# Kernel tuning notes

Measured on AMD Instinct MI355X. Metric: run time of the kernel, lower is better.

## Reference

```python
import jax, jax.numpy as jnp
import numpy as np

EPS = 1e-5  # torch nn.LayerNorm default

def setup_inputs() -> dict:
    key = jax.random.key(0)
    k1, k2 = jax.random.split(key)
    x = jax.random.normal(k1, (8388608, 4), dtype=jnp.float32)
    W = jax.random.normal(k2, (4, 3), dtype=jnp.float32)
    gamma = jnp.ones((4,), dtype=jnp.float32)
    beta = jnp.zeros((4,), dtype=jnp.float32)
    return {"x": x, "W": W, "gamma": gamma, "beta": beta}

def reference(x, W, gamma, beta):
    # LayerNorm over last dim (size 4)
    mu = jnp.mean(x, axis=-1, keepdims=True)
    var = jnp.mean(jnp.square(x - mu), axis=-1, keepdims=True)
    h = (x - mu) * jax.lax.rsqrt(var + EPS) * gamma + beta
    # small linear (4 -> 3) then softmax over last dim
    logits = h @ W  # [N, 3]
    return jax.nn.softmax(logits, axis=-1)
```

## Files before the change

### kernel.cpp

```cpp
#include <hip/hip_runtime.h>

#define LN_EPS 1e-5f

__global__ __launch_bounds__(256) void ln_linear_softmax_kernel(
    const float4* __restrict__ x,
    const float*  __restrict__ W,
    const float*  __restrict__ gamma,
    const float*  __restrict__ beta,
    float*        __restrict__ out,
    int n)
{
    int row = blockIdx.x * blockDim.x + threadIdx.x;
    if (row >= n) return;

    float4 v = x[row];

    float mu = (v.x + v.y + v.z + v.w) * 0.25f;
    float dx = v.x - mu, dy = v.y - mu, dz = v.z - mu, dw = v.w - mu;
    float var = (dx*dx + dy*dy + dz*dz + dw*dw) * 0.25f;
    float rs = rsqrtf(var + LN_EPS);

    float4 g = *(const float4*)gamma;
    float4 b = *(const float4*)beta;
    float h0 = dx * rs * g.x + b.x;
    float h1 = dy * rs * g.y + b.y;
    float h2 = dz * rs * g.z + b.z;
    float h3 = dw * rs * g.w + b.w;

    const float4* W4 = (const float4*)W;
    float4 w0 = W4[0];
    float4 w1 = W4[1];
    float4 w2 = W4[2];

    float l0 = h0*w0.x + h1*w0.w + h2*w1.z + h3*w2.y;
    float l1 = h0*w0.y + h1*w1.x + h2*w1.w + h3*w2.z;
    float l2 = h0*w0.z + h1*w1.y + h2*w2.x + h3*w2.w;

    float m  = fmaxf(l0, fmaxf(l1, l2));
    float e0 = __expf(l0 - m);
    float e1 = __expf(l1 - m);
    float e2 = __expf(l2 - m);
    float inv = 1.0f / (e0 + e1 + e2);

    float* o = out + (size_t)row * 3;
    o[0] = e0 * inv;
    o[1] = e1 * inv;
    o[2] = e2 * inv;
}

extern "C" void kernel_launch(void* const* d_in, const int* in_sizes, int n_in,
                              void* d_out, int out_size, void* d_ws, size_t ws_size,
                              hipStream_t stream) {
    const float* x     = (const float*)d_in[0];
    const float* W     = (const float*)d_in[1];
    const float* gamma = (const float*)d_in[2];
    const float* beta  = (const float*)d_in[3];
    float* out = (float*)d_out;

    int n = in_sizes[0] / 4;
    int block = 256;
    int grid = (n + block - 1) / block;
    ln_linear_softmax_kernel<<<grid, block, 0, stream>>>(
        (const float4*)x, W, gamma, beta, out, n);
}
```

Before: 215.8 us.

## Stage outputs in LDS for coalesced float4 stores, four rows per thread, nontemporal access

Each thread now handles four rows and writes its three softmax outputs into shared memory. After a barrier, the block writes the staged results out as fully coalesced 16-byte nontemporal stores, replacing the scattered 3-float strided stores. Input loads are also marked nontemporal. The aim is to cut partial-cacheline write traffic in this memory-bound kernel. The cost is LDS usage, a barrier, and the requirement that n*3 be divisible by 4 to handle the output tail correctly.

```diff
diff --git a/kernel.cpp b/kernel.cpp
--- a/kernel.cpp
+++ b/kernel.cpp
@@ -2,50 +2,77 @@
 
 #define LN_EPS 1e-5f
 
-__global__ __launch_bounds__(256) void ln_linear_softmax_kernel(
-    const float4* __restrict__ x,
-    const float*  __restrict__ W,
-    const float*  __restrict__ gamma,
-    const float*  __restrict__ beta,
-    float*        __restrict__ out,
+typedef float v4f __attribute__((ext_vector_type(4)));
+
+constexpr int BLOCK = 256;
+constexpr int RPT   = 4;
+constexpr int RPB   = BLOCK * RPT;
+
+__global__ __launch_bounds__(BLOCK) void ln_linear_softmax_kernel(
+    const v4f*   __restrict__ x,
+    const float* __restrict__ W,
+    const float* __restrict__ gamma,
+    const float* __restrict__ beta,
+    v4f*         __restrict__ out4,
     int n)
 {
-    int row = blockIdx.x * blockDim.x + threadIdx.x;
-    if (row >= n) return;
+    __shared__ float lds[RPB * 3];
 
-    float4 v = x[row];
+    const int  tid  = threadIdx.x;
+    const long base = (long)blockIdx.x * RPB;
 
-    float mu = (v.x + v.y + v.z + v.w) * 0.25f;
-    float dx = v.x - mu, dy = v.y - mu, dz = v.z - mu, dw = v.w - mu;
-    float var = (dx*dx + dy*dy + dz*dz + dw*dw) * 0.25f;
-    float rs = rsqrtf(var + LN_EPS);
+    const v4f g = *(const v4f*)gamma;
+    const v4f b = *(const v4f*)beta;
+    const v4f* W4 = (const v4f*)W;
+    const v4f w0 = W4[0];
+    const v4f w1 = W4[1];
+    const v4f w2 = W4[2];
 
-    float4 g = *(const float4*)gamma;
-    float4 b = *(const float4*)beta;
-    float h0 = dx * rs * g.x + b.x;
-    float h1 = dy * rs * g.y + b.y;
-    float h2 = dz * rs * g.z + b.z;
-    float h3 = dw * rs * g.w + b.w;
+    #pragma unroll
+    for (int k = 0; k < RPT; ++k) {
+        const int  rl  = tid + k * BLOCK;
+        const long row = base + rl;
+        if (row < n) {
+            v4f v = __builtin_nontemporal_load(&x[row]);
 
-    const float4* W4 = (const float4*)W;
-    float4 w0 = W4[0];
-    float4 w1 = W4[1];
-    float4 w2 = W4[2];
+            float mu = (v.x + v.y + v.z + v.w) * 0.25f;
+            float dx = v.x - mu, dy = v.y - mu, dz = v.z - mu, dw = v.w - mu;
+            float var = (dx*dx + dy*dy + dz*dz + dw*dw) * 0.25f;
+            float rs  = rsqrtf(var + LN_EPS);
 
-    float l0 = h0*w0.x + h1*w0.w + h2*w1.z + h3*w2.y;
-    float l1 = h0*w0.y + h1*w1.x + h2*w1.w + h3*w2.z;
-    float l2 = h0*w0.z + h1*w1.y + h2*w2.x + h3*w2.w;
+            float h0 = dx * rs * g.x + b.x;
+            float h1 = dy * rs * g.y + b.y;
+            float h2 = dz * rs * g.z + b.z;
+            float h3 = dw * rs * g.w + b.w;
 
-    float m  = fmaxf(l0, fmaxf(l1, l2));
-    float e0 = __expf(l0 - m);
-    float e1 = __expf(l1 - m);
-    float e2 = __expf(l2 - m);
-    float inv = 1.0f / (e0 + e1 + e2);
+            float l0 = h0*w0.x + h1*w0.w + h2*w1.z + h3*w2.y;
+            float l1 = h0*w0.y + h1*w1.x + h2*w1.w + h3*w2.z;
+            float l2 = h0*w0.z + h1*w1.y + h2*w2.x + h3*w2.w;
 
-    float* o = out + (size_t)row * 3;
-    o[0] = e0 * inv;
-    o[1] = e1 * inv;
-    o[2] = e2 * inv;
+            float m   = fmaxf(l0, fmaxf(l1, l2));
+            float e0  = __expf(l0 - m);
+            float e1  = __expf(l1 - m);
+            float e2  = __expf(l2 - m);
+            float inv = 1.0f / (e0 + e1 + e2);
+
+            lds[rl*3 + 0] = e0 * inv;
+            lds[rl*3 + 1] = e1 * inv;
+            lds[rl*3 + 2] = e2 * inv;
+        }
+    }
+
+    __syncthreads();
+
+    const v4f* lds4  = (const v4f*)lds;
+    const long obase = (long)blockIdx.x * (RPB * 3 / 4);
+    const long on4   = ((long)n * 3) / 4;
+    #pragma unroll
+    for (int k = 0; k < 3; ++k) {
+        const long oi = obase + tid + k * BLOCK;
+        if (oi < on4) {
+            __builtin_nontemporal_store(lds4[tid + k * BLOCK], &out4[oi]);
+        }
+    }
 }
 
 extern "C" void kernel_launch(void* const* d_in, const int* in_sizes, int n_in,
@@ -55,11 +82,10 @@
     const float* W     = (const float*)d_in[1];
     const float* gamma = (const float*)d_in[2];
     const float* beta  = (const float*)d_in[3];
-    float* out = (float*)d_out;
+    v4f* out4 = (v4f*)d_out;
 
     int n = in_sizes[0] / 4;
-    int block = 256;
-    int grid = (n + block - 1) / block;
-    ln_linear_softmax_kernel<<<grid, block, 0, stream>>>(
-        (const float4*)x, W, gamma, beta, out, n);
+    int grid = (n + RPB - 1) / RPB;
+    ln_linear_softmax_kernel<<<grid, BLOCK, 0, stream>>>(
+        (const v4f*)x, W, gamma, beta, out4, n);
 }
```

New measurement: 213.3 us. About the same (-1.2%).
